# Kernel tuning notes

Measured on AMD Instinct MI355X. Metric: run time of the kernel, lower is better.

Reference implementation:

```python
import jax, jax.numpy as jnp
import numpy as np

A = -0.75  # PyTorch bicubic convolution constant

def _cubic_weights(t):
    # t: fractional part in [0,1). Returns the 4 tap weights
    # (matches PyTorch get_cubic_upsample_coefficients with A=-0.75).
    t1 = t + 1.0
    w0 = ((A * t1 - 5.0 * A) * t1 + 8.0 * A) * t1 - 4.0 * A
    w1 = ((A + 2.0) * t - (A + 3.0)) * t * t + 1.0
    s = 1.0 - t
    w2 = ((A + 2.0) * s - (A + 3.0)) * s * s + 1.0
    s2 = 2.0 - t
    w3 = ((A * s2 - 5.0 * A) * s2 + 8.0 * A) * s2 - 4.0 * A
    return (w0, w1, w2, w3)

def _reflect_index(i, size):
    # integer reflection for padding_mode='reflection', align_corners=True over [0, size-1]
    span = size - 1
    if span <= 0:
        return jnp.zeros_like(i)
    m = jnp.abs(i) % (2 * span)
    return jnp.where(m > span, 2 * span - m, m)

def _bicubic_warp(x, flow):
    # x: [B,C,H,W], flow: [B,2,H,W] (flow[:,0]=dx, flow[:,1]=dy)
    B, C, H, W = x.shape
    gx = jnp.arange(W, dtype=x.dtype)
    gy = jnp.arange(H, dtype=x.dtype)
    # normalize-to-[-1,1] then grid_sample unnormalize (align_corners=True) cancel exactly:
    ix = gx[None, None, :] + flow[:, 0]  # [B,H,W] source x coord
    iy = gy[None, :, None] + flow[:, 1]  # [B,H,W] source y coord
    bx = jnp.floor(ix)
    by = jnp.floor(iy)
    tx = ix - bx
    ty = iy - by
    bx = bx.astype(jnp.int32)
    by = by.astype(jnp.int32)
    wx = _cubic_weights(tx)
    wy = _cubic_weights(ty)
    xf = x.reshape(B, C, H * W)
    out = jnp.zeros_like(x)
    for j in range(4):  # fixed 4x4 tap stencil
        Y = _reflect_index(by + (j - 1), H)
        for i in range(4):
            X = _reflect_index(bx + (i - 1), W)
            idx = (Y * W + X).reshape(B, 1, H * W)
            v = jnp.take_along_axis(xf, idx, axis=2).reshape(B, C, H, W)
            out = out + v * (wy[j] * wx[i])[:, None]
    return out

def setup_inputs() -> dict:
    key = jax.random.key(0)
    k1, k2, k3 = jax.random.split(key, 3)
    B, C, H, W = 8, 4, 1024, 1024
    return {
        "input": jax.random.normal(k1, (B, C, H, W), dtype=jnp.float32),
        "target": jax.random.normal(k2, (B, C, H, W), dtype=jnp.float32),
        "flow": jax.random.normal(k3, (B, 2, H, W), dtype=jnp.float32),
    }

def reference(input, target, flow):
    warped = _bicubic_warp(target, flow)
    b = 5
    return jnp.mean(jnp.abs(input[..., b:-b, b:-b] - warped[..., b:-b, b:-b]))
```

## Files before the change

kernel.cpp:

```cpp
#include <hip/hip_runtime.h>

constexpr int BB = 8, CC = 4, HH = 1024, WW = 1024, CROP = 5;
constexpr int HC = HH - 2 * CROP, WC = WW - 2 * CROP;
constexpr int HW = HH * WW;
constexpr float AA = -0.75f;

constexpr int NSTRIP = 16;
constexpr int GRID = 32 * NSTRIP * 2;
constexpr int RING = 16;
constexpr int SWID = 272;
constexpr int CH_STRIDE = RING * SWID;

typedef __attribute__((address_space(1))) const void gv_t;
typedef __attribute__((address_space(3))) void lv_t;

__device__ __forceinline__ int reflect_small(int i) {
    int r = i < 0 ? -i : i;
    return r > (HH - 1) ? 2 * (HH - 1) - r : r;
}

__device__ __forceinline__ void cubic_w(float t, float& w0, float& w1,
                                        float& w2, float& w3) {
    float t1 = t + 1.0f;
    w0 = ((AA * t1 - 5.0f * AA) * t1 + 8.0f * AA) * t1 - 4.0f * AA;
    w1 = ((AA + 2.0f) * t - (AA + 3.0f)) * t * t + 1.0f;
    float s = 1.0f - t;
    w2 = ((AA + 2.0f) * s - (AA + 3.0f)) * s * s + 1.0f;
    float s2 = 2.0f - t;
    w3 = ((AA * s2 - 5.0f * AA) * s2 + 8.0f * AA) * s2 - 4.0f * AA;
}

__device__ __noinline__ float px_slow2(const float* __restrict__ tgt_p,
                                       const float* __restrict__ in_p, int pix,
                                       int bx, int by, float wx0, float wx1,
                                       float wx2, float wx3, float wy0,
                                       float wy1, float wy2, float wy3) {
    const int r0 = reflect_small(by - 1) * WW;
    const int r1 = reflect_small(by) * WW;
    const int r2 = reflect_small(by + 1) * WW;
    const int r3 = reflect_small(by + 2) * WW;
    const int c0 = reflect_small(bx - 1);
    const int c1 = reflect_small(bx);
    const int c2 = reflect_small(bx + 1);
    const int c3 = reflect_small(bx + 2);
    float acc = 0.0f;
#pragma unroll
    for (int c = 0; c < 2; ++c) {
        const float* tb = tgt_p + c * HW;
        float q0 = wx0 * tb[r0 + c0] + wx1 * tb[r0 + c1] + wx2 * tb[r0 + c2] +
                   wx3 * tb[r0 + c3];
        float q1 = wx0 * tb[r1 + c0] + wx1 * tb[r1 + c1] + wx2 * tb[r1 + c2] +
                   wx3 * tb[r1 + c3];
        float q2 = wx0 * tb[r2 + c0] + wx1 * tb[r2 + c1] + wx2 * tb[r2 + c2] +
                   wx3 * tb[r2 + c3];
        float q3 = wx0 * tb[r3 + c0] + wx1 * tb[r3 + c1] + wx2 * tb[r3 + c2] +
                   wx3 * tb[r3 + c3];
        float v = wy0 * q0 + wy1 * q1 + wy2 * q2 + wy3 * q3;
        acc += fabsf(in_p[c * HW + pix] - v);
    }
    return acc;
}

__global__ __launch_bounds__(256, 4) void warp_loss_k(
    const float* __restrict__ input, const float* __restrict__ target,
    const float* __restrict__ flow, float* __restrict__ wsbuf) {
    __shared__ float cache[2 * CH_STRIDE];
    const int tid = (int)threadIdx.x;
    const int wv = tid >> 6, lane = tid & 63;

    const int low = (int)blockIdx.x & 511;
    const int pair = (int)blockIdx.x >> 9;
    const int colid = low >> 4;
    const int strip = low & 15;
    const int b = colid >> 2;
    const int chunk = colid & 3;
    const int x0 = CROP + chunk * 256;
    const int wscol = chunk == 0 ? 0 : chunk == 1 ? 252 : chunk == 2 ? 508 : 752;
    const int y0 = CROP + strip * 64;
    const int y1 = min(y0 + 64, CROP + HC);

    const int x = x0 + tid;
    const bool valid_px = x <= 1018;
    const int xc = valid_px ? x : 1018;

    const float* tgt_p = target + (size_t)b * CC * HW + (size_t)(pair * 2) * HW;
    const float* in_p = input + (size_t)b * CC * HW + (size_t)(pair * 2) * HW;
    const float* flow_b = flow + (size_t)b * 2 * HW;

    const int chv = wv >> 1, part = wv & 1;
    const float* plane = tgt_p + (size_t)chv * HW;
    const int chbase = chv * CH_STRIDE;

#pragma unroll 1
    for (int k = 0; k < 12; ++k) {
        const int r = y0 - 5 + k;
        const int slot = r & (RING - 1);
        const float* src = plane + (size_t)r * WW + wscol;
        if (part == 0) {
            __builtin_amdgcn_global_load_lds(
                (gv_t*)(src + lane * 4), (lv_t*)&cache[chbase + slot * SWID],
                16, 0, 0);
        } else {
            __builtin_amdgcn_global_load_lds(
                (gv_t*)(src + 208 + lane),
                (lv_t*)&cache[chbase + slot * SWID + 208], 4, 0, 0);
        }
    }

    float dx0n, dy0n, i00n, i01n, dx1n, dy1n, i10n, i11n;
    {
        const int p0 = y0 * WW + xc;
        const int p1 = (y0 + 1) * WW + xc;
        dx0n = flow_b[p0];
        dy0n = flow_b[HW + p0];
        i00n = in_p[p0];
        i01n = in_p[HW + p0];
        dx1n = flow_b[p1];
        dy1n = flow_b[HW + p1];
        i10n = in_p[p1];
        i11n = in_p[HW + p1];
    }

    __syncthreads();

    float lsum = 0.0f;

    for (int y = y0; y < y1; y += 2) {
        const float dx0 = dx0n, dy0 = dy0n, i00 = i00n, i01 = i01n;
        const float dx1 = dx1n, dy1 = dy1n, i10 = i10n, i11 = i11n;

        {
            const int yn = (y + 2 < y1) ? y + 2 : y;
            const int p0 = yn * WW + xc;
            const int p1 = (yn + 1) * WW + xc;
            dx0n = flow_b[p0];
            dy0n = flow_b[HW + p0];
            i00n = in_p[p0];
            i01n = in_p[HW + p0];
            dx1n = flow_b[p1];
            dy1n = flow_b[HW + p1];
            i10n = in_p[p1];
            i11n = in_p[HW + p1];
        }

#pragma unroll
        for (int rr = 0; rr < 2; ++rr) {
            const int r = y + 7 + rr;
            if (r < HH) {
                const int slot = r & (RING - 1);
                const float* src = plane + (size_t)r * WW + wscol;
                if (part == 0) {
                    __builtin_amdgcn_global_load_lds(
                        (gv_t*)(src + lane * 4),
                        (lv_t*)&cache[chbase + slot * SWID], 16, 0, 0);
                } else {
                    __builtin_amdgcn_global_load_lds(
                        (gv_t*)(src + 208 + lane),
                        (lv_t*)&cache[chbase + slot * SWID + 208], 4, 0, 0);
                }
            }
        }

        {
            const int pix = y * WW + xc;
            const float fx = (float)xc + dx0;
            const float fy = (float)y + dy0;
            const float bxf = floorf(fx), byf = floorf(fy);
            const int bx = (int)bxf, by = (int)byf;
            const float tx = fx - bxf, ty = fy - byf;

            float wx0, wx1, wx2, wx3, wy0, wy1, wy2, wy3;
            cubic_w(tx, wx0, wx1, wx2, wx3);
            cubic_w(ty, wy0, wy1, wy2, wy3);

            const int d = by - y;
            const int cx = bx - 1 - wscol;
            const bool fast =
                valid_px & (d >= -4) & (d <= 4) & (cx >= 0) & (cx <= 268);

            if (fast) {
                const int t = (by - 1) & (RING - 1);
                float v0 = 0.0f, v1 = 0.0f;
#pragma unroll
                for (int j = 0; j < 4; ++j) {
                    const int s = (t + j) & (RING - 1);
                    const int base = s * SWID + cx;
                    const float wyj =
                        j == 0 ? wy0 : j == 1 ? wy1 : j == 2 ? wy2 : wy3;
                    const float* p0 = &cache[base];
                    const float* p1 = &cache[CH_STRIDE + base];
                    v0 += wyj * (p0[0] * wx0 + p0[1] * wx1 + p0[2] * wx2 +
                                 p0[3] * wx3);
                    v1 += wyj * (p1[0] * wx0 + p1[1] * wx1 + p1[2] * wx2 +
                                 p1[3] * wx3);
                }
                lsum += fabsf(i00 - v0) + fabsf(i01 - v1);
            } else if (valid_px) {
                lsum += px_slow2(tgt_p, in_p, pix, bx, by, wx0, wx1, wx2, wx3,
                                 wy0, wy1, wy2, wy3);
            }
        }

        {
            const int yb = y + 1;
            const int pix = yb * WW + xc;
            const float fx = (float)xc + dx1;
            const float fy = (float)yb + dy1;
            const float bxf = floorf(fx), byf = floorf(fy);
            const int bx = (int)bxf, by = (int)byf;
            const float tx = fx - bxf, ty = fy - byf;

            float wx0, wx1, wx2, wx3, wy0, wy1, wy2, wy3;
            cubic_w(tx, wx0, wx1, wx2, wx3);
            cubic_w(ty, wy0, wy1, wy2, wy3);

            const int d = by - yb;
            const int cx = bx - 1 - wscol;
            const bool fast =
                valid_px & (d >= -5) & (d <= 3) & (cx >= 0) & (cx <= 268);

            if (fast) {
                const int t = (by - 1) & (RING - 1);
                float v0 = 0.0f, v1 = 0.0f;
#pragma unroll
                for (int j = 0; j < 4; ++j) {
                    const int s = (t + j) & (RING - 1);
                    const int base = s * SWID + cx;
                    const float wyj =
                        j == 0 ? wy0 : j == 1 ? wy1 : j == 2 ? wy2 : wy3;
                    const float* p0 = &cache[base];
                    const float* p1 = &cache[CH_STRIDE + base];
                    v0 += wyj * (p0[0] * wx0 + p0[1] * wx1 + p0[2] * wx2 +
                                 p0[3] * wx3);
                    v1 += wyj * (p1[0] * wx0 + p1[1] * wx1 + p1[2] * wx2 +
                                 p1[3] * wx3);
                }
                lsum += fabsf(i10 - v0) + fabsf(i11 - v1);
            } else if (valid_px) {
                lsum += px_slow2(tgt_p, in_p, pix, bx, by, wx0, wx1, wx2, wx3,
                                 wy0, wy1, wy2, wy3);
            }
        }

        __syncthreads();
    }

#pragma unroll
    for (int off2 = 32; off2 > 0; off2 >>= 1) lsum += __shfl_down(lsum, off2);

    __shared__ float sm[4];
    if (lane == 0) sm[wv] = lsum;
    __syncthreads();
    if (tid == 0) wsbuf[blockIdx.x] = sm[0] + sm[1] + sm[2] + sm[3];
}

__global__ __launch_bounds__(1024) void reduce_k(const float* __restrict__ ws,
                                                 float* __restrict__ out) {
    float s = 0.0f;
    for (int i = threadIdx.x; i < GRID; i += 1024) s += ws[i];
#pragma unroll
    for (int off = 32; off > 0; off >>= 1) s += __shfl_down(s, off);
    __shared__ float sm[16];
    const int lane = threadIdx.x & 63;
    const int wv = threadIdx.x >> 6;
    if (lane == 0) sm[wv] = s;
    __syncthreads();
    if (threadIdx.x == 0) {
        float t = 0.0f;
#pragma unroll
        for (int i = 0; i < 16; ++i) t += sm[i];
        constexpr float inv_count = 1.0f / ((float)BB * CC * HC * WC);
        out[0] = t * inv_count;
    }
}

extern "C" void kernel_launch(void* const* d_in, const int* in_sizes, int n_in,
                              void* d_out, int out_size, void* d_ws,
                              size_t ws_size, hipStream_t stream) {
    const float* input = (const float*)d_in[0];
    const float* target = (const float*)d_in[1];
    const float* flow = (const float*)d_in[2];
    float* ws = (float*)d_ws;
    float* out = (float*)d_out;

    warp_loss_k<<<GRID, 256, 0, stream>>>(input, target, flow, ws);
    reduce_k<<<1, 1024, 0, stream>>>(ws, out);
}
```

Measured before the change: 109.2 us.

## Use single-wave blocks with private LDS ring and vmcnt waits instead of barriers

Each block becomes one 64-lane wavefront covering a 64-column chunk. It keeps its own 80-wide LDS row ring for both channels, so __syncthreads is replaced by an explicit s_waitcnt vmcnt before reading the cache. The grid grows to 4096 blocks, and the intent is to remove block-wide barrier stalls and let many independent waves overlap memory and compute. The cost is more halo overfetch per column (80 loaded for 64 used). Correctness now relies on the vmcnt count matching the outstanding LDS-load and register-load ordering within the wave.

```diff
diff --git a/kernel.cpp b/kernel.cpp
--- a/kernel.cpp
+++ b/kernel.cpp
@@ -5,11 +5,10 @@
 constexpr int HW = HH * WW;
 constexpr float AA = -0.75f;
 
-constexpr int NSTRIP = 16;
-constexpr int GRID = 32 * NSTRIP * 2;
+constexpr int GRID = 4096;
 constexpr int RING = 16;
-constexpr int SWID = 272;
-constexpr int CH_STRIDE = RING * SWID;
+constexpr int SWID = 80;
+constexpr int CH_W = RING * SWID;
 
 typedef __attribute__((address_space(1))) const void gv_t;
 typedef __attribute__((address_space(3))) void lv_t;
@@ -61,25 +60,24 @@
     return acc;
 }
 
-__global__ __launch_bounds__(256, 4) void warp_loss_k(
+__global__ __launch_bounds__(64, 4) void warp_loss_k(
     const float* __restrict__ input, const float* __restrict__ target,
     const float* __restrict__ flow, float* __restrict__ wsbuf) {
-    __shared__ float cache[2 * CH_STRIDE];
-    const int tid = (int)threadIdx.x;
-    const int wv = tid >> 6, lane = tid & 63;
-
-    const int low = (int)blockIdx.x & 511;
-    const int pair = (int)blockIdx.x >> 9;
-    const int colid = low >> 4;
-    const int strip = low & 15;
-    const int b = colid >> 2;
-    const int chunk = colid & 3;
-    const int x0 = CROP + chunk * 256;
-    const int wscol = chunk == 0 ? 0 : chunk == 1 ? 252 : chunk == 2 ? 508 : 752;
-    const int y0 = CROP + strip * 64;
+    __shared__ float cache[2 * CH_W];
+    const int lane = (int)threadIdx.x;
+    const int g = (int)blockIdx.x;
+    const int pair = g & 1;
+    const int xch = (g >> 1) & 15;
+    const int ystrip = (g >> 5) & 15;
+    const int b = g >> 9;
+
+    const int x0 = CROP + xch * 64;
+    int wsc = (x0 - 8) & ~3;
+    wsc = wsc < 0 ? 0 : (wsc > WW - SWID ? WW - SWID : wsc);
+    const int y0 = CROP + ystrip * 64;
     const int y1 = min(y0 + 64, CROP + HC);
 
-    const int x = x0 + tid;
+    const int x = x0 + lane;
     const bool valid_px = x <= 1018;
     const int xc = valid_px ? x : 1018;
 
@@ -87,23 +85,19 @@
     const float* in_p = input + (size_t)b * CC * HW + (size_t)(pair * 2) * HW;
     const float* flow_b = flow + (size_t)b * 2 * HW;
 
-    const int chv = wv >> 1, part = wv & 1;
-    const float* plane = tgt_p + (size_t)chv * HW;
-    const int chbase = chv * CH_STRIDE;
+    const bool sl = lane < 20;
 
 #pragma unroll 1
     for (int k = 0; k < 12; ++k) {
         const int r = y0 - 5 + k;
         const int slot = r & (RING - 1);
-        const float* src = plane + (size_t)r * WW + wscol;
-        if (part == 0) {
+        if (sl) {
+            const float* s0 = tgt_p + (size_t)r * WW + wsc + lane * 4;
+            __builtin_amdgcn_global_load_lds((gv_t*)s0,
+                                             (lv_t*)&cache[slot * SWID], 16, 0,
+                                             0);
             __builtin_amdgcn_global_load_lds(
-                (gv_t*)(src + lane * 4), (lv_t*)&cache[chbase + slot * SWID],
-                16, 0, 0);
-        } else {
-            __builtin_amdgcn_global_load_lds(
-                (gv_t*)(src + 208 + lane),
-                (lv_t*)&cache[chbase + slot * SWID + 208], 4, 0, 0);
+                (gv_t*)(s0 + HW), (lv_t*)&cache[CH_W + slot * SWID], 16, 0, 0);
         }
     }
 
@@ -121,13 +115,39 @@
         i11n = in_p[HW + p1];
     }
 
-    __syncthreads();
-
     float lsum = 0.0f;
 
     for (int y = y0; y < y1; y += 2) {
         const float dx0 = dx0n, dy0 = dy0n, i00 = i00n, i01 = i01n;
         const float dx1 = dx1n, dy1 = dy1n, i10 = i10n, i11 = i11n;
+
+        {
+            const int r1 = y + 7 > HH - 1 ? HH - 1 : y + 7;
+            const int r2 = y + 8 > HH - 1 ? HH - 1 : y + 8;
+            if (sl) {
+                {
+                    const int slot = r1 & (RING - 1);
+                    const float* s0 = tgt_p + (size_t)r1 * WW + wsc + lane * 4;
+                    __builtin_amdgcn_global_load_lds(
+                        (gv_t*)s0, (lv_t*)&cache[slot * SWID], 16, 0, 0);
+                    __builtin_amdgcn_global_load_lds(
+                        (gv_t*)(s0 + HW), (lv_t*)&cache[CH_W + slot * SWID],
+                        16, 0, 0);
+                }
+                {
+                    const int slot = r2 & (RING - 1);
+                    const float* s0 = tgt_p + (size_t)r2 * WW + wsc + lane * 4;
+                    __builtin_amdgcn_global_load_lds(
+                        (gv_t*)s0, (lv_t*)&cache[slot * SWID], 16, 0, 0);
+                    __builtin_amdgcn_global_load_lds(
+                        (gv_t*)(s0 + HW), (lv_t*)&cache[CH_W + slot * SWID],
+                        16, 0, 0);
+                }
+            }
+        }
+
+        asm volatile("s_waitcnt vmcnt(4)" ::: "memory");
+        __builtin_amdgcn_sched_barrier(0);
 
         {
             const int yn = (y + 2 < y1) ? y + 2 : y;
@@ -143,24 +163,6 @@
             i11n = in_p[HW + p1];
         }
 
-#pragma unroll
-        for (int rr = 0; rr < 2; ++rr) {
-            const int r = y + 7 + rr;
-            if (r < HH) {
-                const int slot = r & (RING - 1);
-                const float* src = plane + (size_t)r * WW + wscol;
-                if (part == 0) {
-                    __builtin_amdgcn_global_load_lds(
-                        (gv_t*)(src + lane * 4),
-                        (lv_t*)&cache[chbase + slot * SWID], 16, 0, 0);
-                } else {
-                    __builtin_amdgcn_global_load_lds(
-                        (gv_t*)(src + 208 + lane),
-                        (lv_t*)&cache[chbase + slot * SWID + 208], 4, 0, 0);
-                }
-            }
-        }
-
         {
             const int pix = y * WW + xc;
             const float fx = (float)xc + dx0;
@@ -174,9 +176,9 @@
             cubic_w(ty, wy0, wy1, wy2, wy3);
 
             const int d = by - y;
-            const int cx = bx - 1 - wscol;
+            const int cx = bx - 1 - wsc;
             const bool fast =
-                valid_px & (d >= -4) & (d <= 4) & (cx >= 0) & (cx <= 268);
+                valid_px & (d >= -4) & (d <= 4) & (cx >= 0) & (cx <= 76);
 
             if (fast) {
                 const int t = (by - 1) & (RING - 1);
@@ -188,7 +190,7 @@
                     const float wyj =
                         j == 0 ? wy0 : j == 1 ? wy1 : j == 2 ? wy2 : wy3;
                     const float* p0 = &cache[base];
-                    const float* p1 = &cache[CH_STRIDE + base];
+                    const float* p1 = &cache[CH_W + base];
                     v0 += wyj * (p0[0] * wx0 + p0[1] * wx1 + p0[2] * wx2 +
                                  p0[3] * wx3);
                     v1 += wyj * (p1[0] * wx0 + p1[1] * wx1 + p1[2] * wx2 +
@@ -200,7 +202,6 @@
                                  wy0, wy1, wy2, wy3);
             }
         }
-
         {
             const int yb = y + 1;
             const int pix = yb * WW + xc;
@@ -215,9 +216,9 @@
             cubic_w(ty, wy0, wy1, wy2, wy3);
 
             const int d = by - yb;
-            const int cx = bx - 1 - wscol;
+            const int cx = bx - 1 - wsc;
             const bool fast =
-                valid_px & (d >= -5) & (d <= 3) & (cx >= 0) & (cx <= 268);
+                valid_px & (d >= -5) & (d <= 3) & (cx >= 0) & (cx <= 76);
 
             if (fast) {
                 const int t = (by - 1) & (RING - 1);
@@ -229,7 +230,7 @@
                     const float wyj =
                         j == 0 ? wy0 : j == 1 ? wy1 : j == 2 ? wy2 : wy3;
                     const float* p0 = &cache[base];
-                    const float* p1 = &cache[CH_STRIDE + base];
+                    const float* p1 = &cache[CH_W + base];
                     v0 += wyj * (p0[0] * wx0 + p0[1] * wx1 + p0[2] * wx2 +
                                  p0[3] * wx3);
                     v1 += wyj * (p1[0] * wx0 + p1[1] * wx1 + p1[2] * wx2 +
@@ -241,17 +242,11 @@
                                  wy0, wy1, wy2, wy3);
             }
         }
-
-        __syncthreads();
     }
 
 #pragma unroll
     for (int off2 = 32; off2 > 0; off2 >>= 1) lsum += __shfl_down(lsum, off2);
-
-    __shared__ float sm[4];
-    if (lane == 0) sm[wv] = lsum;
-    __syncthreads();
-    if (tid == 0) wsbuf[blockIdx.x] = sm[0] + sm[1] + sm[2] + sm[3];
+    if (lane == 0) wsbuf[g] = lsum;
 }
 
 __global__ __launch_bounds__(1024) void reduce_k(const float* __restrict__ ws,
@@ -283,6 +278,6 @@
     float* ws = (float*)d_ws;
     float* out = (float*)d_out;
 
-    warp_loss_k<<<GRID, 256, 0, stream>>>(input, target, flow, ws);
+    warp_loss_k<<<GRID, 64, 0, stream>>>(input, target, flow, ws);
     reduce_k<<<1, 1024, 0, stream>>>(ws, out);
 }
```

After: 112.6 us. 3.1% more time.
